# Performance work log

Hardware: AMD Instinct MI355X
Metric: run time of the kernel (lower is better)

Reference implementation:

```python
import jax, jax.numpy as jnp
import numpy as np

D_MODEL = 1024
D_STATE = 64
N_HEADS = 16
CHUNK = 64


def segsum(x):
    # x: (..., T) -> (..., T, T) with [i, j] = sum_{j<k<=i} x[k], -inf above diagonal
    T = x.shape[-1]
    xx = jnp.broadcast_to(x[..., None], x.shape + (T,))  # [i, j] = x[i]
    lower = jnp.tril(jnp.ones((T, T), dtype=bool), -1)
    xs = jnp.cumsum(jnp.where(lower, xx, 0.0), axis=-2)
    keep = jnp.tril(jnp.ones((T, T), dtype=bool), 0)
    return jnp.where(keep, xs, -jnp.inf)


def ssd_minimal(X, A, B, C, block_len):
    b, L, h, p = X.shape
    n = B.shape[-1]
    c = L // block_len
    l = block_len
    X = X.reshape(b, c, l, h, p)
    A = A.reshape(b, c, l, h).transpose(0, 3, 1, 2)  # b h c l
    B = B.reshape(b, c, l, h, n)
    C = C.reshape(b, c, l, h, n)
    A_cumsum = jnp.cumsum(A, axis=-1)  # b h c l
    Lmat = jnp.exp(segsum(A))  # b h c l l
    Y_diag = jnp.einsum('bclhn,bcshn,bhcls,bcshp->bclhp', C, B, Lmat, X)
    decay_states = jnp.exp(A_cumsum[:, :, :, -1:] - A_cumsum)  # b h c l
    states = jnp.einsum('bclhn,bhcl,bclhp->bchpn', B, decay_states, X)
    init = jnp.zeros_like(states[:, :1])
    states = jnp.concatenate([init, states], axis=1)  # b (c+1) h p n
    A_last = A_cumsum[:, :, :, -1]  # b h c
    decay_chunk = jnp.exp(segsum(jnp.pad(A_last, ((0, 0), (0, 0), (1, 0)))))  # b h (c+1) (c+1)
    new_states = jnp.einsum('bhzc,bchpn->bzhpn', decay_chunk, states)
    states, final_state = new_states[:, :-1], new_states[:, -1]
    state_decay_out = jnp.exp(A_cumsum)  # b h c l
    Y_off = jnp.einsum('bclhn,bchpn,bhcl->bclhp', C, states, state_decay_out)
    Y = (Y_diag + Y_off).reshape(b, L, h, p)
    return Y, final_state


def mamba2_forward(x, W_in, W_dt, b_dt, W_B, W_C, W_out, A_log):
    b, L, d = x.shape
    h, n = N_HEADS, D_STATE
    p = d // h
    # seqlen divisible by CHUNK -> no padding needed (pad_len == 0)
    xz = x @ W_in.T  # (b, L, 2d)
    x_in, z = xz[..., :d], xz[..., d:]
    dt = jax.nn.softplus(x @ W_dt.T + b_dt)  # (b, L, h)
    A = -jnp.exp(A_log)[None, None, :] * dt  # (b, L, h)
    B = (x @ W_B.T).reshape(b, L, h, n)
    C = (x @ W_C.T).reshape(b, L, h, n)
    X = x_in.reshape(b, L, h, p) * dt[..., None]
    Y, new_state = ssd_minimal(X, A, B, C, CHUNK)
    y = Y.reshape(b, L, d) * jax.nn.silu(z)
    y = y @ W_out.T
    return y, new_state


def setup_inputs() -> dict:
    key = jax.random.key(0)
    ks = jax.random.split(key, 7)
    d, h, n = D_MODEL, N_HEADS, D_STATE
    x = jax.random.normal(ks[0], (2, 4096, d), dtype=jnp.float32)
    # xavier_uniform with gain 0.5 for in/out proj
    lim_in = 0.5 * np.sqrt(6.0 / (d + 2 * d))
    W_in = jax.random.uniform(ks[1], (2 * d, d), minval=-lim_in, maxval=lim_in, dtype=jnp.float32)
    lim_out = 0.5 * np.sqrt(6.0 / (d + d))
    W_out = jax.random.uniform(ks[2], (d, d), minval=-lim_out, maxval=lim_out, dtype=jnp.float32)
    # default torch Linear init (kaiming-uniform-ish): U(-1/sqrt(fan_in), 1/sqrt(fan_in))
    lim = 1.0 / np.sqrt(d)
    W_dt = jax.random.uniform(ks[3], (h, d), minval=-lim, maxval=lim, dtype=jnp.float32)
    b_dt = jnp.zeros((h,), dtype=jnp.float32)
    W_B = jax.random.uniform(ks[4], (h * n, d), minval=-lim, maxval=lim, dtype=jnp.float32)
    W_C = jax.random.uniform(ks[5], (h * n, d), minval=-lim, maxval=lim, dtype=jnp.float32)
    A_log = jnp.log(jnp.linspace(1.0, 16.0, h)).astype(jnp.float32)
    return {"x": x, "W_in": W_in, "W_dt": W_dt, "b_dt": b_dt, "W_B": W_B, "W_C": W_C, "W_out": W_out, "A_log": A_log}


def reference(x, W_in, W_dt, b_dt, W_B, W_C, W_out, A_log):
    return mamba2_forward(x, W_in, W_dt, b_dt, W_B, W_C, W_out, A_log)
```

## Files before the change

### kernel.cpp

```cpp
#include <hip/hip_runtime.h>
#include <cstdint>
#include <cstddef>

#define NTOK 8192

typedef __bf16 bf16x8 __attribute__((ext_vector_type(8)));
typedef float f32x4 __attribute__((ext_vector_type(4)));
typedef float f32x4v __attribute__((ext_vector_type(4)));
typedef unsigned short u16x8 __attribute__((ext_vector_type(8)));

__device__ __forceinline__ float b2f(unsigned short u) {
    return __uint_as_float(((unsigned int)u) << 16);
}
__device__ __forceinline__ unsigned short f2b(float f) {
    unsigned int u = __float_as_uint(f);
    u += 0x7FFFu + ((u >> 16) & 1u);
    return (unsigned short)(u >> 16);
}

__device__ __forceinline__ void async_lds16(unsigned short* lds, const unsigned short* g) {
    __builtin_amdgcn_global_load_lds(
        (const __attribute__((address_space(1))) unsigned int*)g,
        (__attribute__((address_space(3))) unsigned int*)lds,
        16, 0, 0);
}

template <int N> __device__ __forceinline__ void waitcnt_vm() {
    if constexpr (N == 8)      asm volatile("s_waitcnt vmcnt(8)" ::: "memory");
    else if constexpr (N == 6) asm volatile("s_waitcnt vmcnt(6)" ::: "memory");
    else                       asm volatile("s_waitcnt vmcnt(0)" ::: "memory");
}

__global__ __launch_bounds__(256) void prep(
    const float* __restrict__ x, const float* __restrict__ W_in,
    const float* __restrict__ W_B, const float* __restrict__ W_C,
    unsigned short* __restrict__ xb, unsigned short* __restrict__ Wst,
    const float* __restrict__ s16a, const float* __restrict__ s16b,
    float* __restrict__ alogf, float* __restrict__ bdtf)
{
    const long i = (long)blockIdx.x * 256 + threadIdx.x;
    const float* src; unsigned short* dst; long off;
    if (i < 1048576)      { src = x;    dst = xb;            off = i; }
    else if (i < 1310720) { src = W_in; dst = Wst;           off = i - 1048576; }
    else if (i < 1441792) { src = W_B;  dst = Wst + 2097152; off = i - 1310720; }
    else if (i < 1572864) { src = W_C;  dst = Wst + 3145728; off = i - 1441792; }
    else {
        if (i == 1572864) {
            float ma = 0.f, mb = 0.f;
            for (int k = 0; k < 16; k++) { ma = fmaxf(ma, fabsf(s16a[k])); mb = fmaxf(mb, fabsf(s16b[k])); }
            const float* alog = (ma >= mb) ? s16a : s16b;
            const float* bdt  = (ma >= mb) ? s16b : s16a;
            for (int k = 0; k < 16; k++) { alogf[k] = alog[k]; bdtf[k] = bdt[k]; }
        }
        return;
    }
    const f32x4v* p = (const f32x4v*)(src + off * 8);
    f32x4v a = p[0], b = p[1];
    u16x8 v;
#pragma unroll
    for (int t = 0; t < 4; t++) { v[t] = f2b(a[t]); v[t + 4] = f2b(b[t]); }
    *(u16x8*)(dst + off * 8) = v;
}

__global__ __launch_bounds__(256) void f32_to_bf16(
    const float* __restrict__ in, unsigned short* __restrict__ out, int n8)
{
    const int i = blockIdx.x * 256 + threadIdx.x;
    if (i >= n8) return;
    const f32x4v* p = (const f32x4v*)(in + (long)i * 8);
    f32x4v a = p[0], b = p[1];
    u16x8 v;
#pragma unroll
    for (int t = 0; t < 4; t++) { v[t] = f2b(a[t]); v[t + 4] = f2b(b[t]); }
    *(u16x8*)(out + (long)i * 8) = v;
}

__global__ __launch_bounds__(256) void dt_kernel(
    const float* __restrict__ x, const float* __restrict__ Wdt,
    const float* __restrict__ bdt, const float* __restrict__ Alog,
    float* __restrict__ dtp, float* __restrict__ Ap)
{
    const int token = blockIdx.x * 16 + (threadIdx.x >> 4);
    const int h = threadIdx.x & 15;
    const f32x4v* xr = (const f32x4v*)(x + (long)token * 1024);
    const f32x4v* wr = (const f32x4v*)(Wdt + h * 1024);
    float s0 = bdt[h], s1 = 0.f;
#pragma unroll 8
    for (int k = 0; k < 256; k += 2) {
        f32x4v a0 = xr[k], w0 = wr[k];
        f32x4v a1 = xr[k + 1], w1 = wr[k + 1];
        s0 += a0[0] * w0[0] + a0[1] * w0[1] + a0[2] * w0[2] + a0[3] * w0[3];
        s1 += a1[0] * w1[0] + a1[1] * w1[1] + a1[2] * w1[2] + a1[3] * w1[3];
    }
    const float s = s0 + s1;
    const float dtv = (s > 15.f) ? s : log1pf(expf(s));
    dtp[token * 16 + h] = dtv;
    Ap[token * 16 + h] = -expf(Alog[h]) * dtv;
}

template <int MODE, int NI>
__global__ __launch_bounds__(512, 2) void gemm256(
    const unsigned short* __restrict__ A, const unsigned short* __restrict__ W,
    const int NT_N, const int N, const int K,
    void* __restrict__ out0, unsigned short* __restrict__ out1,
    unsigned short* __restrict__ out2, unsigned short* __restrict__ out3,
    const float* __restrict__ dtp)
{
    constexpr int BN = NI * 64;
    constexpr int LPS = 4 + NI;

    __shared__ unsigned short As[2][256 * 64];
    __shared__ unsigned short Ws[2][BN * 64];

    const int tid = threadIdx.x;
    const int lane = tid & 63;
    const int warp = tid >> 6;
    const int wm = warp >> 2;
    const int wn = warp & 3;
    const int qm = lane & 15;
    const int quad = lane >> 4;

    const int nwg = gridDim.x;
    const int cpx = nwg >> 3;
    const int bid = blockIdx.x;
    const int swz = (bid & 7) * cpx + (bid >> 3);
    const int bx = swz % NT_N;
    const int by = swz / NT_N;
    const long arow0 = (long)by * 256;
    const long wrow0 = (long)bx * BN;

    const int srow = tid >> 3;
    const int sgc = ((tid & 7) ^ (srow & 7)) * 8;

    f32x4 acc[8][NI];
    const f32x4 zero = {0.f, 0.f, 0.f, 0.f};
#pragma unroll
    for (int i = 0; i < 8; i++)
#pragma unroll
        for (int j = 0; j < NI; j++) acc[i][j] = zero;

    auto stage = [&](int buf, int k0) {
#pragma unroll
        for (int r = 0; r < 4; r++)
            async_lds16(As[buf] + r * 4096 + tid * 8,
                        A + (arow0 + r * 64 + srow) * (long)K + k0 + sgc);
#pragma unroll
        for (int r = 0; r < NI; r++)
            async_lds16(Ws[buf] + r * 4096 + tid * 8,
                        W + (wrow0 + r * 64 + srow) * (long)K + k0 + sgc);
    };
    const int rx = (qm & 7) << 3;
    auto compute = [&](const unsigned short* Ab, const unsigned short* Wb) {
#pragma unroll
        for (int kk = 0; kk < 64; kk += 32) {
            bf16x8 fa[8], fb[NI];
#pragma unroll
            for (int mi = 0; mi < 8; mi++) {
                const int row = wm * 128 + mi * 16 + qm;
                fa[mi] = *(const bf16x8*)(Ab + ((row * 64 + kk + quad * 8) ^ rx));
            }
#pragma unroll
            for (int ni = 0; ni < NI; ni++) {
                const int row = wn * (NI * 16) + ni * 16 + qm;
                fb[ni] = *(const bf16x8*)(Wb + ((row * 64 + kk + quad * 8) ^ rx));
            }
#pragma unroll
            for (int mi = 0; mi < 8; mi++)
#pragma unroll
                for (int ni = 0; ni < NI; ni++)
                    acc[mi][ni] = __builtin_amdgcn_mfma_f32_16x16x32_bf16(
                        fa[mi], fb[ni], acc[mi][ni], 0, 0, 0);
        }
    };

    const int nk = K >> 6;
    stage(0, 0);
    stage(1, 64);
    waitcnt_vm<LPS>();
    __builtin_amdgcn_s_barrier();
    for (int t = 0; t < nk; t++) {
        compute(As[t & 1], Ws[t & 1]);
        if (t + 1 < nk) {
            __builtin_amdgcn_s_barrier();
            if (t + 2 < nk) {
                stage(t & 1, (t + 2) << 6);
                waitcnt_vm<LPS>();
            } else {
                waitcnt_vm<0>();
            }
            __builtin_amdgcn_s_barrier();
        }
    }

#pragma unroll
    for (int mi = 0; mi < 8; mi++)
#pragma unroll
        for (int ni = 0; ni < NI; ni++)
#pragma unroll
            for (int r = 0; r < 4; r++) {
                const long row = arow0 + wm * 128 + mi * 16 + quad * 4 + r;
                const int col = (int)wrow0 + wn * (NI * 16) + ni * 16 + qm;
                const float v = acc[mi][ni][r];
                if (MODE == 0) {
                    ((float*)out0)[row * N + col] = v;
                } else {
                    const int seg = col >> 10, cc = col & 1023;
                    if (seg == 0) {
                        ((unsigned short*)out0)[row * 1024 + cc] = f2b(v * dtp[row * 16 + (cc >> 6)]);
                    } else if (seg == 1) {
                        out1[row * 1024 + cc] = f2b(v / (1.f + expf(-v)));
                    } else if (seg == 2) {
                        out2[row * 1024 + cc] = f2b(v);
                    } else {
                        out3[row * 1024 + cc] = f2b(v);
                    }
                }
            }
}

__global__ __launch_bounds__(256) void ssd_states(
    const unsigned short* __restrict__ Xb, const unsigned short* __restrict__ Bb,
    const float* __restrict__ Ap, float* __restrict__ st_out,
    float* __restrict__ Alast)
{
    __shared__ __align__(16) unsigned short Xh[64 * 64];
    __shared__ __align__(16) unsigned short Xl[64 * 64];
    __shared__ __align__(16) unsigned short Bt[64 * 64];
    __shared__ float dec[64];

    const int blk = blockIdx.x;
    const int h = blk & 15;
    const int c = (blk >> 4) & 63;
    const int b = blk >> 10;
    const long tokenbase = (long)b * 4096 + (long)c * 64;
    const int tid = threadIdx.x;
    const int lane = tid & 63;
    const int w = tid >> 6;
    const int qm = lane & 15;
    const int quad = lane >> 4;

    const int row = tid & 63;
    u16x8 rx[2], rb[2];
#pragma unroll
    for (int i = 0; i < 2; i++) {
        const int ch = (tid >> 6) + 4 * i;
        const long g = (tokenbase + row) * 1024 + h * 64 + ch * 8;
        rx[i] = *(const u16x8*)(Xb + g);
        rb[i] = *(const u16x8*)(Bb + g);
    }
    if (tid < 64) {
        float v = Ap[(tokenbase + tid) * 16 + h];
#pragma unroll
        for (int off = 1; off < 64; off <<= 1) {
            const float u = __shfl_up(v, off, 64);
            if (tid >= off) v += u;
        }
        const float tot = __shfl(v, 63, 64);
        dec[tid] = expf(tot - v);
        if (tid == 63) Alast[(b * 16 + h) * 64 + c] = v;
    }
    __syncthreads();

    const float dv = dec[row];
#pragma unroll
    for (int i = 0; i < 2; i++) {
        const int ch = (tid >> 6) + 4 * i;
#pragma unroll
        for (int t = 0; t < 8; t++) {
            const int pn = ch * 8 + t;
            const int d = (pn * 64 + row) ^ (t << 3);
            const float xd = b2f(rx[i][t]) * dv;
            const unsigned short hi = f2b(xd);
            Xh[d] = hi;
            Xl[d] = f2b(xd - b2f(hi));
            Bt[d] = rb[i][t];
        }
    }
    __syncthreads();

    f32x4 acc[4];
    const f32x4 zero = {0.f, 0.f, 0.f, 0.f};
#pragma unroll
    for (int ni = 0; ni < 4; ni++) acc[ni] = zero;
#pragma unroll
    for (int kk2 = 0; kk2 < 2; kk2++) {
        const int ko = kk2 * 32 + quad * 8;
        const int ra = 16 * w + qm;
        const int da = (ra * 64 + ko) ^ ((ra & 7) << 3);
        bf16x8 fxh = *(const bf16x8*)(Xh + da);
        bf16x8 fxl = *(const bf16x8*)(Xl + da);
#pragma unroll
        for (int ni = 0; ni < 4; ni++) {
            const int rn = ni * 16 + qm;
            bf16x8 fb = *(const bf16x8*)(Bt + ((rn * 64 + ko) ^ ((rn & 7) << 3)));
            acc[ni] = __builtin_amdgcn_mfma_f32_16x16x32_bf16(fxh, fb, acc[ni], 0, 0, 0);
            acc[ni] = __builtin_amdgcn_mfma_f32_16x16x32_bf16(fxl, fb, acc[ni], 0, 0, 0);
        }
    }
    const long sbase = (long)blk * 4096;
    const int p0 = 16 * w + quad * 4;
#pragma unroll
    for (int ni = 0; ni < 4; ni++)
#pragma unroll
        for (int r = 0; r < 4; r++)
            st_out[sbase + (p0 + r) * 64 + ni * 16 + qm] = acc[ni][r];
}

__global__ __launch_bounds__(256) void scan_kernel(
    float* __restrict__ st, const float* __restrict__ Alast)
{
    __shared__ float eal[64];
    const int blk = blockIdx.x;
    const int grp = blk & 15;
    const int h = (blk >> 4) & 15;
    const int b = blk >> 8;
    const int e = grp * 256 + threadIdx.x;
    const float* al = Alast + (b * 16 + h) * 64;
    if (threadIdx.x < 64) eal[threadIdx.x] = expf(al[threadIdx.x]);
    __syncthreads();
    const long base = ((long)(b * 64 * 16 + h)) * 4096 + e;
    const long cstep = (long)16 * 4096;
    float M = 0.f;
    for (int c = 0; c < 64; c += 4) {
        const long i0 = base + (long)c * cstep;
        const float s0 = st[i0];
        const float s1 = st[i0 + cstep];
        const float s2 = st[i0 + 2 * cstep];
        const float s3 = st[i0 + 3 * cstep];
        st[i0] = M;              M = eal[c] * M + s0;
        st[i0 + cstep] = M;      M = eal[c + 1] * M + s1;
        st[i0 + 2 * cstep] = M;  M = eal[c + 2] * M + s2;
        st[i0 + 3 * cstep] = M;  M = eal[c + 3] * M + s3;
    }
    st[(long)8388608 + (long)(b * 16 + h) * 4096 + e] = M;
}

__global__ __launch_bounds__(256) void ssd_yoff(
    const unsigned short* __restrict__ Xb, const unsigned short* __restrict__ Bb,
    const unsigned short* __restrict__ Cb, const float* __restrict__ Ap,
    const float* __restrict__ st, unsigned short* __restrict__ SZb)
{
    __shared__ __align__(16) unsigned short Bs[64 * 64];
    __shared__ __align__(16) unsigned short Ss[64 * 64];
    __shared__ __align__(16) unsigned short Xt[64 * 64];
    __shared__ __align__(16) unsigned short Gs[64 * 64];
    __shared__ float Acum[64];

    const int blk = blockIdx.x;
    const int h = blk & 15;
    const int c = (blk >> 4) & 63;
    const int b = blk >> 10;
    const long tokenbase = (long)b * 4096 + (long)c * 64;
    const int tid = threadIdx.x;
    const int lane = tid & 63;
    const int w = tid >> 6;
    const int qm = lane & 15;
    const int quad = lane >> 4;
    const long sbase = (long)blk * 4096;

    if (tid < 64) {
        float v = Ap[(tokenbase + tid) * 16 + h];
#pragma unroll
        for (int off = 1; off < 64; off <<= 1) {
            const float u = __shfl_up(v, off, 64);
            if (tid >= off) v += u;
        }
        Acum[tid] = v;
    }

#pragma unroll
    for (int i = 0; i < 2; i++) {
        const int idx = tid + i * 256;
        const int r8 = idx >> 3, c8 = (idx & 7) * 8;
        const long g = (tokenbase + r8) * 1024 + h * 64 + c8;
        const int d = (r8 * 64 + c8) ^ ((r8 & 7) << 3);
        *(u16x8*)(Bs + d) = *(const u16x8*)(Bb + g);
        const float* sp = st + sbase + r8 * 64 + c8;
        f32x4v s0 = *(const f32x4v*)sp, s1 = *(const f32x4v*)(sp + 4);
        u16x8 sv;
#pragma unroll
        for (int t = 0; t < 4; t++) { sv[t] = f2b(s0[t]); sv[t + 4] = f2b(s1[t]); }
        *(u16x8*)(Ss + d) = sv;
    }
    const int xrow = tid & 63;
#pragma unroll
    for (int i = 0; i < 2; i++) {
        const int ch = (tid >> 6) + 4 * i;
        const long g = (tokenbase + xrow) * 1024 + h * 64 + ch * 8;
        u16x8 xv = *(const u16x8*)(Xb + g);
#pragma unroll
        for (int t = 0; t < 8; t++) {
            const int p = ch * 8 + t;
            Xt[(p * 64 + xrow) ^ (t << 3)] = xv[t];
        }
    }
    u16x8 fc[2];
#pragma unroll
    for (int kk2 = 0; kk2 < 2; kk2++)
        fc[kk2] = *(const u16x8*)(Cb + (tokenbase + 16 * w + qm) * 1024 + h * 64 + kk2 * 32 + quad * 8);

    __syncthreads();

    f32x4 acc1[4], acc2[4];
    const f32x4 zero = {0.f, 0.f, 0.f, 0.f};
#pragma unroll
    for (int ni = 0; ni < 4; ni++) { acc1[ni] = zero; acc2[ni] = zero; }
#pragma unroll
    for (int kk2 = 0; kk2 < 2; kk2++) {
        const int ko = kk2 * 32 + quad * 8;
        bf16x8 fa = *(const bf16x8*)&fc[kk2];
#pragma unroll
        for (int ni = 0; ni < 4; ni++) {
            const int rn = ni * 16 + qm;
            const int d = (rn * 64 + ko) ^ ((rn & 7) << 3);
            bf16x8 fbb = *(const bf16x8*)(Bs + d);
            acc1[ni] = __builtin_amdgcn_mfma_f32_16x16x32_bf16(fa, fbb, acc1[ni], 0, 0, 0);
            bf16x8 fbs = *(const bf16x8*)(Ss + d);
            acc2[ni] = __builtin_amdgcn_mfma_f32_16x16x32_bf16(fa, fbs, acc2[ni], 0, 0, 0);
        }
    }

    const int l0 = 16 * w + quad * 4;
    float al[4];
#pragma unroll
    for (int r = 0; r < 4; r++) al[r] = Acum[l0 + r];
#pragma unroll
    for (int ni = 0; ni < 4; ni++) {
        const int s = ni * 16 + qm;
        const float as = Acum[s];
#pragma unroll
        for (int r = 0; r < 4; r++) {
            const int l = l0 + r;
            const float gv = (s <= l) ? acc1[ni][r] * expf(al[r] - as) : 0.f;
            Gs[(l * 64 + s) ^ ((l & 7) << 3)] = f2b(gv);
        }
    }
    __syncthreads();

    f32x4 acc3[4];
#pragma unroll
    for (int ni = 0; ni < 4; ni++) acc3[ni] = zero;
#pragma unroll
    for (int kk2 = 0; kk2 < 2; kk2++) {
        const int ko = kk2 * 32 + quad * 8;
        const int ra = 16 * w + qm;
        bf16x8 fg = *(const bf16x8*)(Gs + ((ra * 64 + ko) ^ ((ra & 7) << 3)));
#pragma unroll
        for (int ni = 0; ni < 4; ni++) {
            const int rp = ni * 16 + qm;
            bf16x8 fx = *(const bf16x8*)(Xt + ((rp * 64 + ko) ^ ((rp & 7) << 3)));
            acc3[ni] = __builtin_amdgcn_mfma_f32_16x16x32_bf16(fg, fx, acc3[ni], 0, 0, 0);
        }
    }
    float eds[4];
#pragma unroll
    for (int r = 0; r < 4; r++) eds[r] = expf(al[r]);
#pragma unroll
    for (int ni = 0; ni < 4; ni++) {
#pragma unroll
        for (int r = 0; r < 4; r++) {
            const int l = l0 + r;
            const int p = ni * 16 + qm;
            const float Y = acc3[ni][r] + eds[r] * acc2[ni][r];
            const long o = (tokenbase + l) * 1024 + h * 64 + p;
            SZb[o] = f2b(Y * b2f(SZb[o]));
        }
    }
}

extern "C" void kernel_launch(void* const* d_in, const int* in_sizes, int n_in,
                              void* d_out, int out_size, void* d_ws, size_t ws_size,
                              hipStream_t stream)
{
    int ix = 0, iwin = 1, iwdt = 2, i1m[3] = {4, 5, 6}, n1m = 0, i16[2] = {3, 7}, n16 = 0;
    for (int i = 0; i < n_in; i++) {
        switch (in_sizes[i]) {
            case 8388608: ix = i; break;
            case 2097152: iwin = i; break;
            case 16384:   iwdt = i; break;
            case 1048576: if (n1m < 3) i1m[n1m++] = i; break;
            case 16:      if (n16 < 2) i16[n16++] = i; break;
            default: break;
        }
    }
    if (n1m < 3) { i1m[0] = 4; i1m[1] = 5; i1m[2] = 6; }
    if (n16 < 2) { i16[0] = 3; i16[1] = 7; }
    const float* x     = (const float*)d_in[ix];
    const float* W_in  = (const float*)d_in[iwin];
    const float* W_dt  = (const float*)d_in[iwdt];
    const float* W_B   = (const float*)d_in[i1m[0]];
    const float* W_C   = (const float*)d_in[i1m[1]];
    const float* W_out = (const float*)d_in[i1m[2]];
    const float* s16a  = (const float*)d_in[i16[0]];
    const float* s16b  = (const float*)d_in[i16[1]];
    float* out = (float*)d_out;

    char* ws = (char*)d_ws;
    float* dtp   = (float*)(ws);
    float* Ap    = (float*)(ws + 524288);
    float* Alast = (float*)(ws + 1048576);
    float* Alogf = (float*)(ws + 1056768);
    float* bdtf  = (float*)(ws + 1056832);
    unsigned short* Xb  = (unsigned short*)(ws + 2097152);
    unsigned short* Bb  = (unsigned short*)(ws + 18874368);
    unsigned short* Cb  = (unsigned short*)(ws + 35651584);
    unsigned short* SZb = (unsigned short*)(ws + 52428800);

    unsigned short* xb  = (unsigned short*)d_out;
    unsigned short* Wst = (unsigned short*)((char*)d_out + 16777216);
    unsigned short* Wob = Xb;

    float* states = out;

    prep<<<6145, 256, 0, stream>>>(x, W_in, W_B, W_C, xb, Wst, s16a, s16b, Alogf, bdtf);
    dt_kernel<<<NTOK / 16, 256, 0, stream>>>(x, W_dt, bdtf, Alogf, dtp, Ap);
    gemm256<1, 4><<<512, 512, 0, stream>>>(xb, Wst, 16, 4096, 1024, Xb, SZb, Bb, Cb, dtp);
    ssd_states<<<2048, 256, 0, stream>>>(Xb, Bb, Ap, states, Alast);
    scan_kernel<<<512, 256, 0, stream>>>(states, Alast);
    ssd_yoff<<<2048, 256, 0, stream>>>(Xb, Bb, Cb, Ap, states, SZb);
    f32_to_bf16<<<512, 256, 0, stream>>>(W_out, Wob, 131072);
    gemm256<0, 2><<<256, 512, 0, stream>>>(SZb, Wob, 8, 1024, 1024, out, nullptr, nullptr, nullptr, nullptr);
}
```

Baseline: 357.3 us.

## Add 8-phase interleaved in-projection GEMM overlapping async loads with MFMA

Replaces the in-projection GEMM (8192x4096x1024) with a new kernel that splits each 64-wide K step into two 32-wide halves. Each half has two MFMA phases, and the next tile's async global-to-LDS loads are issued between the LDS reads and the MFMAs, with raised wave priority around the MFMA blocks. The goal is to hide global-load latency and LDS traffic behind matrix math. The cost is many more barriers per K step, and the stage and wait ordering must be exactly right to avoid races. The output GEMM keeps the old kernel with its epilogue simplified.

```diff
diff --git a/kernel.cpp b/kernel.cpp
--- a/kernel.cpp
+++ b/kernel.cpp
@@ -28,6 +28,7 @@
 template <int N> __device__ __forceinline__ void waitcnt_vm() {
     if constexpr (N == 8)      asm volatile("s_waitcnt vmcnt(8)" ::: "memory");
     else if constexpr (N == 6) asm volatile("s_waitcnt vmcnt(6)" ::: "memory");
+    else if constexpr (N == 4) asm volatile("s_waitcnt vmcnt(4)" ::: "memory");
     else                       asm volatile("s_waitcnt vmcnt(0)" ::: "memory");
 }
 
@@ -98,12 +99,141 @@
     Ap[token * 16 + h] = -expf(Alog[h]) * dtv;
 }
 
+__global__ __launch_bounds__(512, 2) void gemm8p(
+    const unsigned short* __restrict__ A, const unsigned short* __restrict__ W,
+    const int NT_N, const int K,
+    unsigned short* __restrict__ out0, unsigned short* __restrict__ out1,
+    unsigned short* __restrict__ out2, unsigned short* __restrict__ out3,
+    const float* __restrict__ dtp)
+{
+    __shared__ unsigned short As[2][2][8192];
+    __shared__ unsigned short Ws[2][2][8192];
+
+    const int tid = threadIdx.x;
+    const int lane = tid & 63;
+    const int warp = tid >> 6;
+    const int wm = warp >> 2;
+    const int wn = warp & 3;
+    const int qm = lane & 15;
+    const int quad = lane >> 4;
+
+    const int nwg = gridDim.x;
+    const int cpx = nwg >> 3;
+    const int bid = blockIdx.x;
+    const int swz = (bid & 7) * cpx + (bid >> 3);
+    const int bx = swz % NT_N;
+    const int by = swz / NT_N;
+    const long arow0 = (long)by * 256;
+    const long wrow0 = (long)bx * 256;
+
+    const int srow2 = tid >> 2;
+    const int sg2 = ((tid & 3) ^ (srow2 & 3)) * 8;
+    const int rgo = (quad ^ (qm & 3)) * 8;
+
+    f32x4 acc[8][4];
+    const f32x4 zero = {0.f, 0.f, 0.f, 0.f};
+#pragma unroll
+    for (int i = 0; i < 8; i++)
+#pragma unroll
+        for (int j = 0; j < 4; j++) acc[i][j] = zero;
+
+    auto stA = [&](int buf, int kh, int k0) {
+#pragma unroll
+        for (int i = 0; i < 2; i++)
+            async_lds16(&As[buf][kh][(i * 512 + tid) * 8],
+                        A + (arow0 + i * 128 + srow2) * (long)K + k0 + kh * 32 + sg2);
+    };
+    auto stW = [&](int buf, int kh, int k0) {
+#pragma unroll
+        for (int i = 0; i < 2; i++)
+            async_lds16(&Ws[buf][kh][(i * 512 + tid) * 8],
+                        W + (wrow0 + i * 128 + srow2) * (long)K + k0 + kh * 32 + sg2);
+    };
+
+    bf16x8 fa[4], fb[4];
+    auto dsA4 = [&](int p, int kh, int mb) {
+#pragma unroll
+        for (int m = 0; m < 4; m++)
+            fa[m] = *(const bf16x8*)(&As[p][kh][(wm * 128 + (mb + m) * 16 + qm) * 32 + rgo]);
+    };
+    auto dsW4 = [&](int p, int kh) {
+#pragma unroll
+        for (int n = 0; n < 4; n++)
+            fb[n] = *(const bf16x8*)(&Ws[p][kh][(wn * 64 + n * 16 + qm) * 32 + rgo]);
+    };
+    auto mf16 = [&](int mb) {
+        __builtin_amdgcn_s_setprio(1);
+#pragma unroll
+        for (int m = 0; m < 4; m++)
+#pragma unroll
+            for (int n = 0; n < 4; n++)
+                acc[mb + m][n] = __builtin_amdgcn_mfma_f32_16x16x32_bf16(
+                    fa[m], fb[n], acc[mb + m][n], 0, 0, 0);
+        __builtin_amdgcn_s_setprio(0);
+    };
+
+    const int nk = K >> 6;
+    stA(0, 0, 0); stW(0, 0, 0); stA(0, 1, 0); stW(0, 1, 0);
+    waitcnt_vm<4>();
+    __builtin_amdgcn_s_barrier();
+    for (int t = 0; t < nk; ++t) {
+        const int p = t & 1;
+        const bool pref = (t + 1 < nk);
+        const int k1 = (t + 1) << 6;
+        dsA4(p, 0, 0); dsW4(p, 0);
+        if (pref) stA(p ^ 1, 0, k1);
+        __builtin_amdgcn_s_barrier();
+        asm volatile("s_waitcnt lgkmcnt(0)" ::: "memory");
+        mf16(0);
+        __builtin_amdgcn_s_barrier();
+        dsA4(p, 0, 4);
+        if (pref) { stW(p ^ 1, 0, k1); waitcnt_vm<4>(); }
+        else waitcnt_vm<0>();
+        __builtin_amdgcn_s_barrier();
+        asm volatile("s_waitcnt lgkmcnt(0)" ::: "memory");
+        mf16(4);
+        __builtin_amdgcn_s_barrier();
+        dsA4(p, 1, 0); dsW4(p, 1);
+        if (pref) stA(p ^ 1, 1, k1);
+        __builtin_amdgcn_s_barrier();
+        asm volatile("s_waitcnt lgkmcnt(0)" ::: "memory");
+        mf16(0);
+        __builtin_amdgcn_s_barrier();
+        dsA4(p, 1, 4);
+        if (pref) { stW(p ^ 1, 1, k1); waitcnt_vm<4>(); }
+        __builtin_amdgcn_s_barrier();
+        asm volatile("s_waitcnt lgkmcnt(0)" ::: "memory");
+        mf16(4);
+        __builtin_amdgcn_s_barrier();
+    }
+
+#pragma unroll
+    for (int mi = 0; mi < 8; mi++)
+#pragma unroll
+        for (int ni = 0; ni < 4; ni++)
+#pragma unroll
+            for (int r = 0; r < 4; r++) {
+                const long row = arow0 + wm * 128 + mi * 16 + quad * 4 + r;
+                const int col = (int)wrow0 + wn * 64 + ni * 16 + qm;
+                const float v = acc[mi][ni][r];
+                const int seg = col >> 10, cc = col & 1023;
+                if (seg == 0) {
+                    out0[row * 1024 + cc] = f2b(v * dtp[row * 16 + (cc >> 6)]);
+                } else if (seg == 1) {
+                    out1[row * 1024 + cc] = f2b(v / (1.f + expf(-v)));
+                } else if (seg == 2) {
+                    out2[row * 1024 + cc] = f2b(v);
+                } else {
+                    out3[row * 1024 + cc] = f2b(v);
+                }
+            }
+}
+
 template <int MODE, int NI>
 __global__ __launch_bounds__(512, 2) void gemm256(
     const unsigned short* __restrict__ A, const unsigned short* __restrict__ W,
     const int NT_N, const int N, const int K,
-    void* __restrict__ out0, unsigned short* __restrict__ out1,
-    unsigned short* __restrict__ out2, unsigned short* __restrict__ out3,
+    void* __restrict__ out0,
     const float* __restrict__ dtp)
 {
     constexpr int BN = NI * 64;
@@ -200,21 +330,7 @@
             for (int r = 0; r < 4; r++) {
                 const long row = arow0 + wm * 128 + mi * 16 + quad * 4 + r;
                 const int col = (int)wrow0 + wn * (NI * 16) + ni * 16 + qm;
-                const float v = acc[mi][ni][r];
-                if (MODE == 0) {
-                    ((float*)out0)[row * N + col] = v;
-                } else {
-                    const int seg = col >> 10, cc = col & 1023;
-                    if (seg == 0) {
-                        ((unsigned short*)out0)[row * 1024 + cc] = f2b(v * dtp[row * 16 + (cc >> 6)]);
-                    } else if (seg == 1) {
-                        out1[row * 1024 + cc] = f2b(v / (1.f + expf(-v)));
-                    } else if (seg == 2) {
-                        out2[row * 1024 + cc] = f2b(v);
-                    } else {
-                        out3[row * 1024 + cc] = f2b(v);
-                    }
-                }
+                ((float*)out0)[row * N + col] = acc[mi][ni][r];
             }
 }
 
@@ -514,10 +630,10 @@
 
     prep<<<6145, 256, 0, stream>>>(x, W_in, W_B, W_C, xb, Wst, s16a, s16b, Alogf, bdtf);
     dt_kernel<<<NTOK / 16, 256, 0, stream>>>(x, W_dt, bdtf, Alogf, dtp, Ap);
-    gemm256<1, 4><<<512, 512, 0, stream>>>(xb, Wst, 16, 4096, 1024, Xb, SZb, Bb, Cb, dtp);
+    gemm8p<<<512, 512, 0, stream>>>(xb, Wst, 16, 1024, Xb, SZb, Bb, Cb, dtp);
     ssd_states<<<2048, 256, 0, stream>>>(Xb, Bb, Ap, states, Alast);
     scan_kernel<<<512, 256, 0, stream>>>(states, Alast);
     ssd_yoff<<<2048, 256, 0, stream>>>(Xb, Bb, Cb, Ap, states, SZb);
     f32_to_bf16<<<512, 256, 0, stream>>>(W_out, Wob, 131072);
-    gemm256<0, 2><<<256, 512, 0, stream>>>(SZb, Wob, 8, 1024, 1024, out, nullptr, nullptr, nullptr, nullptr);
-}
+    gemm256<0, 2><<<256, 512, 0, stream>>>(SZb, Wob, 8, 1024, 1024, out, nullptr);
+}
```

Measured after the change: 386.4 us. 1.08x slower.
